# Performance work log

Hardware: AMD Instinct MI355X
Metric: run time of the kernel (lower is better)

## Reference

```python
import jax, jax.numpy as jnp
import numpy as np

N, E, D = 50000, 800000, 128
BN_EPS = 1e-5


def mish(x):
    return x * jnp.tanh(jax.nn.softplus(x))


def setup_inputs() -> dict:
    key = jax.random.key(0)
    ks = jax.random.split(key, 16)
    s = 1.0 / np.sqrt(D)
    s2 = 1.0 / np.sqrt(2 * D)
    # unique (row, col) edge pairs so the dense-adjacency edge norm reduces
    # exactly to conv_w[bond_type] + conv_b per edge
    rng = np.random.default_rng(0)
    codes = np.unique(rng.integers(0, N * N, size=2 * E, dtype=np.int64))[:E]
    edge_index = jnp.asarray(np.stack([codes // N, codes % N]), dtype=jnp.int32)
    bond_types = jnp.asarray(rng.integers(0, 4, size=E), dtype=jnp.int32)

    def nrm(k, shape, sc):
        return jax.random.normal(k, shape, jnp.float32) * sc

    return {
        "x": nrm(ks[0], (N, D), 1.0),
        "coords": nrm(ks[1], (N, 3), 1.0),
        "edge_index": edge_index,
        "bond_types": bond_types,
        # NodeFeaturePath
        "W_nb": nrm(ks[2], (2 * D, D), s2), "b_nb": jnp.zeros((D,), jnp.float32),
        "W_nout": nrm(ks[3], (D, D), s), "b_nout": jnp.zeros((D,), jnp.float32),
        # EdgeFeaturePath (1x1 conv over 4 bond-type channels -> scalar per edge)
        "conv_w": nrm(ks[4], (4,), 0.5), "conv_b": jnp.zeros((), jnp.float32),
        "W_el": nrm(ks[5], (2 * D, D), s2), "b_el": jnp.zeros((D,), jnp.float32),
        "W_eout": nrm(ks[6], (D, D), s), "b_eout": jnp.zeros((D,), jnp.float32),
        # StructuralFeaturePath
        "W_coord": nrm(ks[7], (2 * D, D), s2), "b_coord": jnp.zeros((D,), jnp.float32),
        "W_pair": nrm(ks[8], (D, D), s), "b_pair": jnp.zeros((D,), jnp.float32),
        "W_sout": nrm(ks[9], (2 * D, D), s2), "b_sout": jnp.zeros((D,), jnp.float32),
        # FeatureAggregation (att mode, all bias-free)
        "W_init": nrm(ks[10], (D, D), s),
        "feat_lin": nrm(ks[11], (3, D, D), s),
        "W_att": nrm(ks[12], (2 * D, D), s2),
        "W_agg": nrm(ks[13], (D, D), s),
        # BatchNorm (training mode)
        "gamma": jnp.ones((D,), jnp.float32), "beta": jnp.zeros((D,), jnp.float32),
    }


def _forward(x, coords, edge_index, bond_types,
             W_nb, b_nb, W_nout, b_nout,
             conv_w, conv_b, W_el, b_el, W_eout, b_eout,
             W_coord, b_coord, W_pair, b_pair, W_sout, b_sout,
             W_init, feat_lin, W_att, W_agg, gamma, beta):
    act = mish
    src, dst = edge_index[0], edge_index[1]  # PyG: x_j = x[src], x_i = x[dst]
    pair = jnp.concatenate([x[dst], x[src]], axis=1)  # [E, 2D] = [x_i, x_j]

    # --- node path ---
    msg = act(pair @ W_nb + b_nb)                                  # [E, D]
    P = jax.ops.segment_sum(msg, dst, num_segments=N)              # [N, D]
    f_node = act(P @ W_nout + b_nout)

    # --- edge path: 1x1 conv over one-hot bond-type adjacency == lookup ---
    norm_e = (conv_w[bond_types] + conv_b)[:, None]                # [E, 1]
    msg = act((norm_e * pair) @ W_el + b_el)
    P = jax.ops.segment_sum(msg, dst, num_segments=N)
    f_edge = act(P @ W_eout + b_eout)

    # --- struct path ---
    d2 = jnp.sum((coords[src] - coords[dst]) ** 2, axis=1, keepdims=True)  # [E,1]
    msg = (d2 * pair) @ W_coord + b_coord                          # no act in message
    Q = jax.ops.segment_sum(msg, dst, num_segments=N)
    Q = act(Q @ W_pair + b_pair)
    f_struct = act(jnp.concatenate([x, Q], axis=1) @ W_sout + b_sout)

    # --- attention aggregation over the 3 feature paths ---
    feat_stack = jnp.stack([f_node, f_edge, f_struct], axis=0)     # [3, N, D]
    lin_init = act(x @ W_init)[None]                               # [1, N, D] (broadcast of repeat)
    lin_feats = act(jnp.einsum('fnd,fde->fne', feat_stack, feat_lin))
    h = act(jnp.concatenate([jnp.broadcast_to(lin_init, lin_feats.shape), lin_feats], axis=2))
    e = h @ W_att                                                  # [3, N, D]
    a = jax.nn.softmax(e, axis=0)
    att = jnp.sum(a * feat_stack, axis=0)                          # einsum fnd,fnd->nd
    h_agg = att @ W_agg

    # --- batchnorm (training stats, biased var) + final activation ---
    mean = h_agg.mean(axis=0)
    var = h_agg.var(axis=0)
    h_bn = (h_agg - mean) / jnp.sqrt(var + BN_EPS) * gamma + beta
    return act(h_bn)  # final=False


def reference(x, coords, edge_index, bond_types,
              W_nb, b_nb, W_nout, b_nout,
              conv_w, conv_b, W_el, b_el, W_eout, b_eout,
              W_coord, b_coord, W_pair, b_pair, W_sout, b_sout,
              W_init, feat_lin, W_att, W_agg, gamma, beta):
    return _forward(x, coords, edge_index, bond_types,
                    W_nb, b_nb, W_nout, b_nout,
                    conv_w, conv_b, W_el, b_el, W_eout, b_eout,
                    W_coord, b_coord, W_pair, b_pair, W_sout, b_sout,
                    W_init, feat_lin, W_att, W_agg, gamma, beta)
```

## Files before the change

kernel.cpp:

```cpp
#include <hip/hip_runtime.h>
#include <math.h>

#define DD 128
#define LDSS 136
#define PLANE (16 * LDSS)
#define WT 16384

typedef __attribute__((ext_vector_type(8))) short bf16x8;
typedef __attribute__((ext_vector_type(4))) float f32x4;
typedef unsigned short u16;
typedef unsigned int u32;

__device__ __forceinline__ u16 f2bf(float f) {
    u32 u = __builtin_bit_cast(u32, f);
    u += 0x7fffu + ((u >> 16) & 1u);
    return (u16)(u >> 16);
}
__device__ __forceinline__ float bf2f(u16 h) {
    u32 u = ((u32)h) << 16;
    return __builtin_bit_cast(float, u);
}
__device__ __forceinline__ float mishf(float x) {
    float e = __expf(fminf(x, 15.0f));
    float n = e * (e + 2.0f);
    return x * n * __builtin_amdgcn_rcpf(n + 2.0f);
}
__device__ __forceinline__ void splitv(float v, u16& h, u16& l) {
    u32 u = __builtin_bit_cast(u32, v);
    h = (u16)(u >> 16);
    float r = v - __builtin_bit_cast(float, u & 0xffff0000u);
    l = (u16)(__builtin_bit_cast(u32, r) >> 16);
}

template<int NM>
__device__ __forceinline__ void gemm2(const bf16x8* ah, const bf16x8* al,
    const u16* __restrict__ Wh, const u16* __restrict__ Wl, int lane, int ntB, f32x4* acc)
{
#pragma unroll
    for (int kb = 0; kb < 4; kb++)
#pragma unroll
        for (int j = 0; j < 2; j++) {
            size_t boff = (((size_t)kb * 8 + ntB + j) * 64 + lane) * 8;
            bf16x8 bh = *(const bf16x8*)(Wh + boff);
            acc[j] = __builtin_amdgcn_mfma_f32_16x16x32_bf16(ah[kb], bh, acc[j], 0, 0, 0);
            if (NM >= 2) {
                bf16x8 bl = *(const bf16x8*)(Wl + boff);
                acc[j] = __builtin_amdgcn_mfma_f32_16x16x32_bf16(ah[kb], bl, acc[j], 0, 0, 0);
            }
            if (NM == 3)
                acc[j] = __builtin_amdgcn_mfma_f32_16x16x32_bf16(al[kb], bh, acc[j], 0, 0, 0);
        }
}

__device__ __forceinline__ void gemm2_dual(const bf16x8* a1, const bf16x8* a2,
    const u16* __restrict__ W1h, const u16* __restrict__ W1l,
    const u16* __restrict__ W2h, const u16* __restrict__ W2l,
    int lane, int ntB, f32x4* acc1, f32x4* acc2)
{
#pragma unroll
    for (int kb = 0; kb < 4; kb++)
#pragma unroll
        for (int j = 0; j < 2; j++) {
            size_t boff = (((size_t)kb * 8 + ntB + j) * 64 + lane) * 8;
            bf16x8 b1h = *(const bf16x8*)(W1h + boff);
            bf16x8 b1l = *(const bf16x8*)(W1l + boff);
            acc1[j] = __builtin_amdgcn_mfma_f32_16x16x32_bf16(a1[kb], b1h, acc1[j], 0, 0, 0);
            acc1[j] = __builtin_amdgcn_mfma_f32_16x16x32_bf16(a1[kb], b1l, acc1[j], 0, 0, 0);
            bf16x8 b2h = (W2h == W1h) ? b1h : *(const bf16x8*)(W2h + boff);
            bf16x8 b2l = (W2l == W1l) ? b1l : *(const bf16x8*)(W2l + boff);
            acc2[j] = __builtin_amdgcn_mfma_f32_16x16x32_bf16(a2[kb], b2h, acc2[j], 0, 0, 0);
            acc2[j] = __builtin_amdgcn_mfma_f32_16x16x32_bf16(a2[kb], b2l, acc2[j], 0, 0, 0);
        }
}

__device__ __forceinline__ void zero2(f32x4* acc) {
    f32x4 z4 = {0.f, 0.f, 0.f, 0.f};
    acc[0] = z4; acc[1] = z4;
}

__device__ __forceinline__ void frag_hi_global16(const u16* __restrict__ src, int row0,
                                                 int lm, int quad, int M, bf16x8* ah)
{
    int row = row0 + lm; if (row >= M) row = M - 1;
    const u16* p = src + (size_t)row * DD + quad * 8;
#pragma unroll
    for (int kb = 0; kb < 4; kb++) ah[kb] = *(const bf16x8*)(p + kb * 32);
}
__device__ __forceinline__ void frag_split_global16(const float* __restrict__ src, int row0,
                                                    int lm, int quad, int M, bf16x8* ah, bf16x8* al)
{
    int row = row0 + lm; if (row >= M) row = M - 1;
    const float* p = src + (size_t)row * DD + quad * 8;
#pragma unroll
    for (int kb = 0; kb < 4; kb++) {
        float tmp[8];
        *(float4*)tmp       = *(const float4*)(p + kb * 32);
        *(float4*)(tmp + 4) = *(const float4*)(p + kb * 32 + 4);
#pragma unroll
        for (int j = 0; j < 8; j++) { u16 h, l; splitv(tmp[j], h, l); ah[kb][j] = (short)h; al[kb][j] = (short)l; }
    }
}
__device__ __forceinline__ void frag_hi_plane16(const u16* P, int lm, int quad, bf16x8* ah)
{
    const u16* p = P + (size_t)lm * LDSS + quad * 8;
#pragma unroll
    for (int kb = 0; kb < 4; kb++) ah[kb] = *(const bf16x8*)(p + kb * 32);
}
__device__ __forceinline__ void frag_planes16(const u16* PH, const u16* PL, int lm, int quad,
                                              bf16x8* ah, bf16x8* al)
{
    const u16* ph = PH + (size_t)lm * LDSS + quad * 8;
    const u16* pl = PL + (size_t)lm * LDSS + quad * 8;
#pragma unroll
    for (int kb = 0; kb < 4; kb++) {
        ah[kb] = *(const bf16x8*)(ph + kb * 32);
        al[kb] = *(const bf16x8*)(pl + kb * 32);
    }
}

struct WSrc { const float* p[18]; };

__global__ __launch_bounds__(256) void prep_weights(WSrc ws, u16* __restrict__ Wh, u16* __restrict__ Wl)
{
    int mat = blockIdx.x >> 3, chunk = blockIdx.x & 7;
    int t = threadIdx.x;
    int tt = chunk * 4 + (t >> 6);
    int lane = t & 63;
    int kb = tt >> 3, nt = tt & 7;
    const float* __restrict__ src = ws.p[mat];
    size_t doff = (size_t)mat * WT + ((size_t)tt * 64 + lane) * 8;
    int srow = kb * 32 + ((lane >> 4) * 8);
    int scol = nt * 16 + (lane & 15);
    u16 th[8], tl[8];
#pragma unroll
    for (int j = 0; j < 8; j++) {
        float v = src[(srow + j) * DD + scol];
        u16 h = f2bf(v);
        th[j] = h;
        tl[j] = f2bf(v - bf2f(h));
    }
    *(bf16x8*)(Wh + doff) = *(bf16x8*)th;
    *(bf16x8*)(Wl + doff) = *(bf16x8*)tl;
}

__global__ __launch_bounds__(256, 4) void fronthist_kernel(
    const float* __restrict__ x, const u16* __restrict__ Wh, const u16* __restrict__ Wl,
    u16* __restrict__ G, u16* __restrict__ xWs,
    float* __restrict__ At, float* __restrict__ Bt, float* __restrict__ Ct,
    const int* __restrict__ ei, int* __restrict__ deg, int E, int M, int NBF)
{
    __shared__ u16 sP[3 * PLANE];
    const int t = threadIdx.x;
    if ((int)blockIdx.x >= NBF) {
        int e = ((int)blockIdx.x - NBF) * 256 + t;
        if (e < E) atomicAdd(&deg[ei[E + e]], 1);
        return;
    }
    u16 *P0 = sP, *P1 = sP + PLANE, *P2 = sP + 2 * PLANE;
    const int wave = t >> 6, lane = t & 63;
    const int lm = lane & 15, quad = lane >> 4;
    const int ntB = wave * 2;
    const int row0 = blockIdx.x * 16;

    bf16x8 ah[4], al[4];
    {
        int row = row0 + lm; if (row >= M) row = M - 1;
        const float* p = x + (size_t)row * DD + quad * 8;
#pragma unroll
        for (int kb = 0; kb < 4; kb++) {
            float tmp[8];
            *(float4*)tmp       = *(const float4*)(p + kb * 32);
            *(float4*)(tmp + 4) = *(const float4*)(p + kb * 32 + 4);
#pragma unroll
            for (int j = 0; j < 8; j++) {
                u16 h, l; splitv(tmp[j], h, l);
                ah[kb][j] = (short)h; al[kb][j] = (short)l;
                if (wave == 0) P0[lm * LDSS + kb * 32 + quad * 8 + j] = f2bf(tmp[j]);
            }
        }
    }
    {
        f32x4 acc[2]; zero2(acc);
        gemm2<1>(ah, ah, Wh + 1 * WT, Wh, lane, ntB, acc);
#pragma unroll
        for (int r = 0; r < 4; r++)
#pragma unroll
            for (int j = 0; j < 2; j++)
                P1[(quad * 4 + r) * LDSS + (ntB + j) * 16 + lm] = f2bf(acc[j][r]);
    }
    {
        f32x4 acc[2]; zero2(acc);
        gemm2<1>(ah, ah, Wh + 3 * WT, Wh, lane, ntB, acc);
#pragma unroll
        for (int r = 0; r < 4; r++)
#pragma unroll
            for (int j = 0; j < 2; j++)
                P2[(quad * 4 + r) * LDSS + (ntB + j) * 16 + lm] = f2bf(acc[j][r]);
    }
    __syncthreads();
#pragma unroll
    for (int i = 0; i < 4; i++) {
        int r = wave * 4 + i;
        int grow = row0 + r;
        if (grow >= M) continue;
        u16* gp = G + (size_t)grow * 384;
        *(u32*)(gp +       lane * 2) = *(const u32*)&P1[r * LDSS + lane * 2];
        *(u32*)(gp + 128 + lane * 2) = *(const u32*)&P2[r * LDSS + lane * 2];
        *(u32*)(gp + 256 + lane * 2) = *(const u32*)&P0[r * LDSS + lane * 2];
    }
    {
        f32x4 acc[2]; zero2(acc);
        gemm2<1>(ah, ah, Wh + 5 * WT, Wh, lane, ntB, acc);
#pragma unroll
        for (int r = 0; r < 4; r++) {
            int grow = row0 + quad * 4 + r;
            if (grow >= M) continue;
#pragma unroll
            for (int j = 0; j < 2; j++)
                xWs[(size_t)grow * DD + (ntB + j) * 16 + lm] = f2bf(acc[j][r]);
        }
    }
    {
        float* outs[3] = {At, Bt, Ct};
        const int mats[3] = {0, 2, 4};
#pragma unroll
        for (int wi = 0; wi < 3; wi++) {
            f32x4 acc[2]; zero2(acc);
            gemm2<3>(ah, al, Wh + (size_t)mats[wi] * WT, Wl + (size_t)mats[wi] * WT, lane, ntB, acc);
            float* out = outs[wi];
#pragma unroll
            for (int r = 0; r < 4; r++) {
                int grow = row0 + quad * 4 + r;
                if (grow >= M) continue;
#pragma unroll
                for (int j = 0; j < 2; j++)
                    out[(size_t)grow * DD + (ntB + j) * 16 + lm] = acc[j][r];
            }
        }
    }
}

__global__ __launch_bounds__(1024) void scan_kernel(const int* __restrict__ deg,
                                                    int* __restrict__ rowptr,
                                                    int* __restrict__ cursor, int N)
{
    __shared__ int sums[1024];
    const int CH = 52;
    int t = threadIdx.x;
    int base = t * CH;
    int local = 0;
#pragma unroll
    for (int i = 0; i < 13; i++) {
        int idx = base + i * 4;
        if (idx + 3 < N) {
            int4 v = *(const int4*)(deg + idx);
            local += v.x + v.y + v.z + v.w;
        } else {
            for (int k = 0; k < 4; k++) if (idx + k < N) local += deg[idx + k];
        }
    }
    sums[t] = local;
    __syncthreads();
    for (int off = 1; off < 1024; off <<= 1) {
        int v = sums[t];
        int u = (t >= off) ? sums[t - off] : 0;
        __syncthreads();
        sums[t] = v + u;
        __syncthreads();
    }
    int run = (t == 0) ? 0 : sums[t - 1];
    for (int i = 0; i < CH; i++) {
        int idx = base + i;
        if (idx < N) {
            rowptr[idx] = run;
            cursor[idx] = run;
            run += deg[idx];
        }
    }
    if (t == 1023) rowptr[N] = sums[1023];
}

__global__ __launch_bounds__(256) void scatter_kernel(
    const int* __restrict__ ei, const int* __restrict__ bond,
    const float* __restrict__ coords, int* __restrict__ cursor,
    int2* __restrict__ csr, int E)
{
    int e = blockIdx.x * 256 + threadIdx.x;
    if (e >= E) return;
    int src = ei[e], dst = ei[E + e];
    int pos = atomicAdd(&cursor[dst], 1);
    float dx = coords[src * 3 + 0] - coords[dst * 3 + 0];
    float dy = coords[src * 3 + 1] - coords[dst * 3 + 1];
    float dz = coords[src * 3 + 2] - coords[dst * 3 + 2];
    float d2 = dx * dx + dy * dy + dz * dz;
    csr[pos] = make_int2(src | (bond[e] << 20), __float_as_int(d2));
}

__global__ __launch_bounds__(256) void edge_agg(
    const float* __restrict__ At, const float* __restrict__ Bt,
    const u16* __restrict__ G,
    const int* __restrict__ rowptr, const int2* __restrict__ csr,
    const float* __restrict__ conv_w, const float* __restrict__ conv_b,
    const float* __restrict__ b_nb, const float* __restrict__ b_el,
    u16* __restrict__ Pn, u16* __restrict__ Pe, float* __restrict__ z,
    float* __restrict__ s_arr, int N)
{
    int wave = threadIdx.x >> 6;
    int lane = threadIdx.x & 63;
    int node = blockIdx.x * 4 + wave;
    if (node >= N) return;
    int c0 = lane * 2;
    float2 at = *(const float2*)(At + (size_t)node * DD + c0);
    float2 bt = *(const float2*)(Bt + (size_t)node * DD + c0);
    float cb = conv_b[0];
    float cw0 = conv_w[0] + cb, cw1 = conv_w[1] + cb, cw2 = conv_w[2] + cb, cw3 = conv_w[3] + cb;
    float bn0 = b_nb[c0], bn1 = b_nb[c0 + 1];
    float be0 = b_el[c0], be1 = b_el[c0 + 1];
    float accn0 = 0.f, accn1 = 0.f, acce0 = 0.f, acce1 = 0.f, accz0 = 0.f, accz1 = 0.f, ssum = 0.f;
    int beg = rowptr[node], end = rowptr[node + 1];

    auto consume = [&](int px, float d2, u32 ga, u32 gb, u32 gx) {
        int bondv = (px >> 20) & 3;
        float w = (bondv == 0) ? cw0 : (bondv == 1) ? cw1 : (bondv == 2) ? cw2 : cw3;
        float a0 = __builtin_bit_cast(float, ga << 16), a1 = __builtin_bit_cast(float, ga & 0xffff0000u);
        float b0 = __builtin_bit_cast(float, gb << 16), b1 = __builtin_bit_cast(float, gb & 0xffff0000u);
        float x0 = __builtin_bit_cast(float, gx << 16), x1 = __builtin_bit_cast(float, gx & 0xffff0000u);
        accn0 += mishf(at.x + a0 + bn0);
        accn1 += mishf(at.y + a1 + bn1);
        acce0 += mishf(w * (bt.x + b0) + be0);
        acce1 += mishf(w * (bt.y + b1) + be1);
        accz0 += d2 * x0;
        accz1 += d2 * x1;
        ssum += d2;
    };

    int k = beg;
    for (; k + 4 <= end; k += 4) {
        int2 pd0 = csr[k], pd1 = csr[k + 1], pd2 = csr[k + 2], pd3 = csr[k + 3];
        const u16* g0 = G + (size_t)(pd0.x & 0xFFFFF) * 384;
        const u16* g1 = G + (size_t)(pd1.x & 0xFFFFF) * 384;
        const u16* g2 = G + (size_t)(pd2.x & 0xFFFFF) * 384;
        const u16* g3 = G + (size_t)(pd3.x & 0xFFFFF) * 384;
        u32 ga0 = *(const u32*)(g0 + c0), gb0 = *(const u32*)(g0 + 128 + c0), gx0 = *(const u32*)(g0 + 256 + c0);
        u32 ga1 = *(const u32*)(g1 + c0), gb1 = *(const u32*)(g1 + 128 + c0), gx1 = *(const u32*)(g1 + 256 + c0);
        u32 ga2 = *(const u32*)(g2 + c0), gb2 = *(const u32*)(g2 + 128 + c0), gx2 = *(const u32*)(g2 + 256 + c0);
        u32 ga3 = *(const u32*)(g3 + c0), gb3 = *(const u32*)(g3 + 128 + c0), gx3 = *(const u32*)(g3 + 256 + c0);
        consume(pd0.x, __int_as_float(pd0.y), ga0, gb0, gx0);
        consume(pd1.x, __int_as_float(pd1.y), ga1, gb1, gx1);
        consume(pd2.x, __int_as_float(pd2.y), ga2, gb2, gx2);
        consume(pd3.x, __int_as_float(pd3.y), ga3, gb3, gx3);
    }
    for (; k < end; k++) {
        int2 pd = csr[k];
        const u16* gp = G + (size_t)(pd.x & 0xFFFFF) * 384;
        u32 ga = *(const u32*)(gp + c0);
        u32 gb = *(const u32*)(gp + 128 + c0);
        u32 gx = *(const u32*)(gp + 256 + c0);
        consume(pd.x, __int_as_float(pd.y), ga, gb, gx);
    }

    *(u32*)(Pn + (size_t)node * DD + c0) = (u32)f2bf(accn0) | ((u32)f2bf(accn1) << 16);
    *(u32*)(Pe + (size_t)node * DD + c0) = (u32)f2bf(acce0) | ((u32)f2bf(acce1) << 16);
    *(float2*)(z + (size_t)node * DD + c0) = make_float2(accz0, accz1);
    if (lane == 0) s_arr[node] = ssum;
}

__global__ __launch_bounds__(256, 4) void mega_kernel(
    const u16* __restrict__ Pn, const u16* __restrict__ Pe, const float* __restrict__ z,
    const float* __restrict__ Ct, const u16* __restrict__ xWs,
    const float* __restrict__ s_arr, const int* __restrict__ deg,
    const float* __restrict__ b_nout, const float* __restrict__ b_eout,
    const float* __restrict__ b_coord, const float* __restrict__ b_pair,
    const float* __restrict__ b_sout,
    const u16* __restrict__ Wh, const u16* __restrict__ Wl,
    float* __restrict__ hout, float* __restrict__ bnsums, int M)
{
    __shared__ u16 sP[4 * PLANE];
    u16 *PA = sP, *PB = sP + PLANE, *PC = sP + 2 * PLANE, *PD = sP + 3 * PLANE;
    const int t = threadIdx.x, wave = t >> 6, lane = t & 63;
    const int lm = lane & 15, quad = lane >> 4;
    const int ntB = wave * 2;
    const int row0 = blockIdx.x * 16;

    u32 f1p[4], f2p[4], f3p[4];
    float d1v[8], d2v[8];

    {
        bf16x8 an[4], ae[4];
        f32x4 accn[2], acce[2];
        frag_hi_global16(Pn, row0, lm, quad, M, an);
        frag_hi_global16(Pe, row0, lm, quad, M, ae);
        zero2(accn); zero2(acce);
        gemm2_dual(an, ae, Wh + 11 * WT, Wl + 11 * WT, Wh + 12 * WT, Wl + 12 * WT, lane, ntB, accn, acce);
#pragma unroll
        for (int r = 0; r < 4; r++) {
            u32 pkn = 0, pke = 0;
#pragma unroll
            for (int j = 0; j < 2; j++) {
                int col = (ntB + j) * 16 + lm;
                int lidx = (quad * 4 + r) * LDSS + col;
                u16 hn = f2bf(mishf(accn[j][r] + b_nout[col]));
                u16 he = f2bf(mishf(acce[j][r] + b_eout[col]));
                pkn |= ((u32)hn) << (16 * j);
                pke |= ((u32)he) << (16 * j);
                PA[lidx] = hn; PB[lidx] = he;
            }
            f1p[r] = pkn; f2p[r] = pke;
        }
        __syncthreads();
        frag_hi_plane16(PA, lm, quad, an);
        frag_hi_plane16(PB, lm, quad, ae);
        zero2(accn); zero2(acce);
        gemm2_dual(an, ae, Wh + 13 * WT, Wl + 13 * WT, Wh + 14 * WT, Wl + 14 * WT, lane, ntB, accn, acce);
#pragma unroll
        for (int r = 0; r < 4; r++)
#pragma unroll
            for (int j = 0; j < 2; j++) {
                int lidx = (quad * 4 + r) * LDSS + (ntB + j) * 16 + lm;
                PC[lidx] = f2bf(mishf(mishf(accn[j][r])));
                PD[lidx] = f2bf(mishf(mishf(acce[j][r])));
            }
        __syncthreads();
        frag_hi_plane16(PC, lm, quad, an);
        frag_hi_plane16(PD, lm, quad, ae);
        zero2(accn); zero2(acce);
        gemm2_dual(an, ae, Wh + 16 * WT, Wl + 16 * WT, Wh + 16 * WT, Wl + 16 * WT, lane, ntB, accn, acce);
#pragma unroll
        for (int r = 0; r < 4; r++)
#pragma unroll
            for (int j = 0; j < 2; j++) {
                d1v[r * 2 + j] = accn[j][r];
                d2v[r * 2 + j] = acce[j][r];
            }
    }

    bf16x8 ah[4], al[4];
    f32x4 acc[2];
    frag_split_global16(z, row0, lm, quad, M, ah, al);
    zero2(acc);
    gemm2<3>(ah, al, Wh + 8 * WT, Wl + 8 * WT, lane, ntB, acc);
#pragma unroll
    for (int r = 0; r < 4; r++) {
        int crow = row0 + quad * 4 + r; if (crow >= M) crow = M - 1;
        float sv = s_arr[crow];
        float dv = (float)deg[crow];
#pragma unroll
        for (int j = 0; j < 2; j++) {
            int col = (ntB + j) * 16 + lm;
            float v = acc[j][r] + sv * Ct[(size_t)crow * DD + col] + dv * b_coord[col];
            int lidx = (quad * 4 + r) * LDSS + col;
            u16 h, l; splitv(v, h, l); PA[lidx] = h; PB[lidx] = l;
        }
    }
    __syncthreads();
    frag_planes16(PA, PB, lm, quad, ah, al);
    zero2(acc);
    gemm2<3>(ah, al, Wh + 9 * WT, Wl + 9 * WT, lane, ntB, acc);
#pragma unroll
    for (int r = 0; r < 4; r++)
#pragma unroll
        for (int j = 0; j < 2; j++) {
            int col = (ntB + j) * 16 + lm;
            int lidx = (quad * 4 + r) * LDSS + col;
            u16 h, l; splitv(mishf(acc[j][r] + b_pair[col]), h, l); PC[lidx] = h; PD[lidx] = l;
        }
    __syncthreads();
    frag_planes16(PC, PD, lm, quad, ah, al);
    zero2(acc);
    gemm2<3>(ah, al, Wh + 10 * WT, Wl + 10 * WT, lane, ntB, acc);
#pragma unroll
    for (int r = 0; r < 4; r++) {
        int crow = row0 + quad * 4 + r; if (crow >= M) crow = M - 1;
        u32 pk = 0;
#pragma unroll
        for (int j = 0; j < 2; j++) {
            int col = (ntB + j) * 16 + lm;
            float v = mishf(acc[j][r] + bf2f(xWs[(size_t)crow * DD + col]) + b_sout[col]);
            u16 h, l; splitv(v, h, l);
            pk |= ((u32)f2bf(v)) << (16 * j);
            int lidx = (quad * 4 + r) * LDSS + col;
            PA[lidx] = h; PB[lidx] = l;
        }
        f3p[r] = pk;
    }
    __syncthreads();
    frag_planes16(PA, PB, lm, quad, ah, al);
    zero2(acc);
    gemm2<3>(ah, al, Wh + 15 * WT, Wl + 15 * WT, lane, ntB, acc);
#pragma unroll
    for (int r = 0; r < 4; r++)
#pragma unroll
        for (int j = 0; j < 2; j++) {
            int lidx = (quad * 4 + r) * LDSS + (ntB + j) * 16 + lm;
            u16 h, l; splitv(mishf(mishf(acc[j][r])), h, l); PC[lidx] = h; PD[lidx] = l;
        }
    __syncthreads();
    frag_planes16(PC, PD, lm, quad, ah, al);
    zero2(acc);
    gemm2<3>(ah, al, Wh + 16 * WT, Wl + 16 * WT, lane, ntB, acc);

#pragma unroll
    for (int r = 0; r < 4; r++)
#pragma unroll
        for (int j = 0; j < 2; j++) {
            int i = r * 2 + j;
            float x1 = d1v[i], x2 = d2v[i], x3 = acc[j][r];
            float m = fmaxf(fmaxf(x1, x2), x3);
            float p1 = __expf(x1 - m), p2 = __expf(x2 - m), p3 = __expf(x3 - m);
            float fv1 = bf2f((u16)(f1p[r] >> (16 * j)));
            float fv2 = bf2f((u16)(f2p[r] >> (16 * j)));
            float fv3 = bf2f((u16)(f3p[r] >> (16 * j)));
            float att = (p1 * fv1 + p2 * fv2 + p3 * fv3) * __builtin_amdgcn_rcpf(p1 + p2 + p3);
            int lidx = (quad * 4 + r) * LDSS + (ntB + j) * 16 + lm;
            u16 h, l; splitv(att, h, l); PA[lidx] = h; PB[lidx] = l;
        }
    __syncthreads();
    frag_planes16(PA, PB, lm, quad, ah, al);
    zero2(acc);
    gemm2<3>(ah, al, Wh + 17 * WT, Wl + 17 * WT, lane, ntB, acc);
    float s[2] = {0.f, 0.f}, q[2] = {0.f, 0.f};
#pragma unroll
    for (int r = 0; r < 4; r++) {
        int grow = row0 + quad * 4 + r;
        if (grow >= M) continue;
#pragma unroll
        for (int j = 0; j < 2; j++) {
            float v = acc[j][r];
            hout[(size_t)grow * DD + (ntB + j) * 16 + lm] = v;
            s[j] += v; q[j] += v * v;
        }
    }
    __syncthreads();
    float* red = (float*)sP;
    if (t < 128) { red[t] = 0.f; red[128 + t] = 0.f; }
    __syncthreads();
#pragma unroll
    for (int j = 0; j < 2; j++) {
        int col = (ntB + j) * 16 + lm;
        atomicAdd(&red[col], s[j]);
        atomicAdd(&red[128 + col], q[j]);
    }
    __syncthreads();
    if (t < 128) {
        atomicAdd(&bnsums[t], red[t]);
        atomicAdd(&bnsums[128 + t], red[128 + t]);
    }
}

__global__ void bn_finalize(const float* __restrict__ sums, const float* __restrict__ gamma,
                            const float* __restrict__ beta, float* __restrict__ scale,
                            float* __restrict__ shift, float n_inv)
{
    int c = threadIdx.x;
    float mean = sums[c] * n_inv;
    float var = sums[128 + c] * n_inv - mean * mean;
    float inv = rsqrtf(var + 1e-5f);
    float sc = gamma[c] * inv;
    scale[c] = sc;
    shift[c] = beta[c] - mean * sc;
}

__global__ __launch_bounds__(256) void bn_apply(float* __restrict__ h, const float* __restrict__ scale,
                                                const float* __restrict__ shift, size_t total4)
{
    size_t idx = (size_t)blockIdx.x * 256 + threadIdx.x;
    if (idx >= total4) return;
    size_t off = idx * 4;
    int c = (int)(off & 127);
    float4 v = *(const float4*)(h + off);
    float4 sc = *(const float4*)(scale + c);
    float4 sh = *(const float4*)(shift + c);
    v.x = mishf(v.x * sc.x + sh.x);
    v.y = mishf(v.y * sc.y + sh.y);
    v.z = mishf(v.z * sc.z + sh.z);
    v.w = mishf(v.w * sc.w + sh.w);
    *(float4*)(h + off) = v;
}

extern "C" void kernel_launch(void* const* d_in, const int* in_sizes, int n_in,
                              void* d_out, int out_size, void* d_ws, size_t ws_size,
                              hipStream_t stream)
{
    (void)n_in; (void)out_size; (void)ws_size;
    const float* x       = (const float*)d_in[0];
    const float* coords  = (const float*)d_in[1];
    const int*   ei      = (const int*)d_in[2];
    const int*   bond    = (const int*)d_in[3];
    const float* W_nb    = (const float*)d_in[4];
    const float* b_nb    = (const float*)d_in[5];
    const float* W_nout  = (const float*)d_in[6];
    const float* b_nout  = (const float*)d_in[7];
    const float* conv_w  = (const float*)d_in[8];
    const float* conv_b  = (const float*)d_in[9];
    const float* W_el    = (const float*)d_in[10];
    const float* b_el    = (const float*)d_in[11];
    const float* W_eout  = (const float*)d_in[12];
    const float* b_eout  = (const float*)d_in[13];
    const float* W_coord = (const float*)d_in[14];
    const float* b_coord = (const float*)d_in[15];
    const float* W_pair  = (const float*)d_in[16];
    const float* b_pair  = (const float*)d_in[17];
    const float* W_sout  = (const float*)d_in[18];
    const float* b_sout  = (const float*)d_in[19];
    const float* W_init  = (const float*)d_in[20];
    const float* feat_lin= (const float*)d_in[21];
    const float* W_att   = (const float*)d_in[22];
    const float* W_agg   = (const float*)d_in[23];
    const float* gamma   = (const float*)d_in[24];
    const float* beta    = (const float*)d_in[25];

    const int N = in_sizes[0] / DD;
    const int E = in_sizes[3];
    const size_t ND = (size_t)N * DD;
    const int SUB = DD * DD;
    const int NB16 = (N + 15) / 16;
    const int EB   = (E + 255) / 256;

    char* base = (char*)d_ws;
    size_t off = 0;
    auto alloc = [&](size_t bytes) -> char* {
        char* p = base + off;
        off = (off + bytes + 63) & ~(size_t)63;
        return p;
    };
    u16*   G    = (u16*)alloc((size_t)N * 384 * 2);
    u16*   xWs  = (u16*)alloc(ND * 2);
    float* At   = (float*)alloc(ND * 4);
    float* Bt   = (float*)alloc(ND * 4);
    float* Ct   = (float*)alloc(ND * 4);
    u16*   Pn   = (u16*)alloc(ND * 2);
    u16*   Pe   = (u16*)alloc(ND * 2);
    float* z    = (float*)alloc(ND * 4);
    u16*   Wh   = (u16*)alloc((size_t)18 * WT * 2);
    u16*   Wl   = (u16*)alloc((size_t)18 * WT * 2);
    int2*  csr  = (int2*)alloc((size_t)E * 8);
    int*   deg    = (int*)alloc((size_t)(N + 64) * 4);
    int*   rowptr = (int*)alloc((size_t)(N + 1) * 4);
    int*   cursor = (int*)alloc((size_t)N * 4);
    float* s_arr  = (float*)alloc((size_t)N * 4);
    float* bnsums  = (float*)alloc(256 * 4);
    float* bnscale = (float*)alloc(128 * 4);
    float* bnshift = (float*)alloc(128 * 4);

    float* hout = (float*)d_out;

    WSrc wsrc;
    wsrc.p[0] = W_nb;            wsrc.p[1] = W_nb + SUB;
    wsrc.p[2] = W_el;            wsrc.p[3] = W_el + SUB;
    wsrc.p[4] = W_coord;         wsrc.p[5] = W_sout;
    wsrc.p[6] = W_init;          wsrc.p[7] = W_att;
    wsrc.p[8] = W_coord + SUB;   wsrc.p[9] = W_pair;
    wsrc.p[10] = W_sout + SUB;   wsrc.p[11] = W_nout;
    wsrc.p[12] = W_eout;         wsrc.p[13] = feat_lin;
    wsrc.p[14] = feat_lin + SUB; wsrc.p[15] = feat_lin + 2 * SUB;
    wsrc.p[16] = W_att + SUB;    wsrc.p[17] = W_agg;

    const dim3 blk256(256);
    const size_t total4 = ND / 4;
    const dim3 gElem((unsigned)((total4 + 255) / 256));

    hipMemsetAsync(deg, 0, (size_t)N * 4, stream);
    hipMemsetAsync(bnsums, 0, 256 * 4, stream);

    prep_weights<<<dim3(18 * 8), blk256, 0, stream>>>(wsrc, Wh, Wl);
    fronthist_kernel<<<dim3(NB16 + EB), blk256, 0, stream>>>(x, Wh, Wl, G, xWs, At, Bt, Ct,
                                                             ei, deg, E, N, NB16);
    scan_kernel<<<1, 1024, 0, stream>>>(deg, rowptr, cursor, N);
    scatter_kernel<<<dim3(EB), blk256, 0, stream>>>(ei, bond, coords, cursor, csr, E);

    edge_agg<<<(N + 3) / 4, blk256, 0, stream>>>(At, Bt, G, rowptr, csr, conv_w, conv_b,
                                                 b_nb, b_el, Pn, Pe, z, s_arr, N);

    mega_kernel<<<NB16, blk256, 0, stream>>>(Pn, Pe, z, Ct, xWs, s_arr, deg,
                                             b_nout, b_eout, b_coord, b_pair, b_sout,
                                             Wh, Wl, hout, bnsums, N);

    bn_finalize<<<1, 128, 0, stream>>>(bnsums, gamma, beta, bnscale, bnshift, 1.0f / (float)N);
    bn_apply<<<gElem, blk256, 0, stream>>>(hout, bnscale, bnshift, total4);
}
```

Baseline: 613.8 us.

## Split node edges across two waves and add dual-accumulator MFMA chains

edge_agg now gives each node two waves that take alternating edges and combine their partial sums through shared memory, doubling the waves available to hide gather latency. Chosen GEMMs in mega_kernel use a second accumulator for odd k-blocks to break the serial MFMA dependency chain. mega_kernel's launch-bounds occupancy hint drops from 4 to 3 to leave room for the extra accumulator registers. Costs are a block-wide barrier, an LDS reduction in edge_agg, and possibly lower occupancy in mega_kernel.

New measurement: 623.0 us. Within noise of the previous version (+1.5%).

```diff
diff --git a/kernel.cpp b/kernel.cpp
--- a/kernel.cpp
+++ b/kernel.cpp
@@ -32,24 +32,36 @@
     l = (u16)(__builtin_bit_cast(u32, r) >> 16);
 }
 
-template<int NM>
+__device__ __forceinline__ void zero2(f32x4* acc) {
+    f32x4 z4 = {0.f, 0.f, 0.f, 0.f};
+    acc[0] = z4; acc[1] = z4;
+}
+
+template<int NM, bool SPLIT = false>
 __device__ __forceinline__ void gemm2(const bf16x8* ah, const bf16x8* al,
     const u16* __restrict__ Wh, const u16* __restrict__ Wl, int lane, int ntB, f32x4* acc)
 {
+    f32x4 accB[2];
+    if (SPLIT) zero2(accB);
 #pragma unroll
     for (int kb = 0; kb < 4; kb++)
 #pragma unroll
         for (int j = 0; j < 2; j++) {
             size_t boff = (((size_t)kb * 8 + ntB + j) * 64 + lane) * 8;
+            f32x4* ac = (SPLIT && (kb & 1)) ? accB : acc;
             bf16x8 bh = *(const bf16x8*)(Wh + boff);
-            acc[j] = __builtin_amdgcn_mfma_f32_16x16x32_bf16(ah[kb], bh, acc[j], 0, 0, 0);
+            ac[j] = __builtin_amdgcn_mfma_f32_16x16x32_bf16(ah[kb], bh, ac[j], 0, 0, 0);
             if (NM >= 2) {
                 bf16x8 bl = *(const bf16x8*)(Wl + boff);
-                acc[j] = __builtin_amdgcn_mfma_f32_16x16x32_bf16(ah[kb], bl, acc[j], 0, 0, 0);
+                ac[j] = __builtin_amdgcn_mfma_f32_16x16x32_bf16(ah[kb], bl, ac[j], 0, 0, 0);
             }
             if (NM == 3)
-                acc[j] = __builtin_amdgcn_mfma_f32_16x16x32_bf16(al[kb], bh, acc[j], 0, 0, 0);
-        }
+                ac[j] = __builtin_amdgcn_mfma_f32_16x16x32_bf16(al[kb], bh, ac[j], 0, 0, 0);
+        }
+    if (SPLIT) {
+        acc[0] += accB[0];
+        acc[1] += accB[1];
+    }
 }
 
 __device__ __forceinline__ void gemm2_dual(const bf16x8* a1, const bf16x8* a2,
@@ -73,11 +85,6 @@
         }
 }
 
-__device__ __forceinline__ void zero2(f32x4* acc) {
-    f32x4 z4 = {0.f, 0.f, 0.f, 0.f};
-    acc[0] = z4; acc[1] = z4;
-}
-
 __device__ __forceinline__ void frag_hi_global16(const u16* __restrict__ src, int row0,
                                                  int lm, int quad, int M, bf16x8* ah)
 {
@@ -305,19 +312,24 @@
     u16* __restrict__ Pn, u16* __restrict__ Pe, float* __restrict__ z,
     float* __restrict__ s_arr, int N)
 {
+    __shared__ float part[2][7][64];
     int wave = threadIdx.x >> 6;
     int lane = threadIdx.x & 63;
-    int node = blockIdx.x * 4 + wave;
-    if (node >= N) return;
+    int p = wave >> 1;
+    int s = wave & 1;
+    int node = blockIdx.x * 2 + p;
+    bool valid = node < N;
+    int nclamp = valid ? node : N - 1;
     int c0 = lane * 2;
-    float2 at = *(const float2*)(At + (size_t)node * DD + c0);
-    float2 bt = *(const float2*)(Bt + (size_t)node * DD + c0);
+    float2 at = *(const float2*)(At + (size_t)nclamp * DD + c0);
+    float2 bt = *(const float2*)(Bt + (size_t)nclamp * DD + c0);
     float cb = conv_b[0];
     float cw0 = conv_w[0] + cb, cw1 = conv_w[1] + cb, cw2 = conv_w[2] + cb, cw3 = conv_w[3] + cb;
     float bn0 = b_nb[c0], bn1 = b_nb[c0 + 1];
     float be0 = b_el[c0], be1 = b_el[c0 + 1];
     float accn0 = 0.f, accn1 = 0.f, acce0 = 0.f, acce1 = 0.f, accz0 = 0.f, accz1 = 0.f, ssum = 0.f;
-    int beg = rowptr[node], end = rowptr[node + 1];
+    int beg = 0, end = 0;
+    if (valid) { beg = rowptr[node]; end = rowptr[node + 1]; }
 
     auto consume = [&](int px, float d2, u32 ga, u32 gb, u32 gx) {
         int bondv = (px >> 20) & 3;
@@ -334,9 +346,9 @@
         ssum += d2;
     };
 
-    int k = beg;
-    for (; k + 4 <= end; k += 4) {
-        int2 pd0 = csr[k], pd1 = csr[k + 1], pd2 = csr[k + 2], pd3 = csr[k + 3];
+    int k = beg + s;
+    for (; k + 6 < end; k += 8) {
+        int2 pd0 = csr[k], pd1 = csr[k + 2], pd2 = csr[k + 4], pd3 = csr[k + 6];
         const u16* g0 = G + (size_t)(pd0.x & 0xFFFFF) * 384;
         const u16* g1 = G + (size_t)(pd1.x & 0xFFFFF) * 384;
         const u16* g2 = G + (size_t)(pd2.x & 0xFFFFF) * 384;
@@ -350,7 +362,7 @@
         consume(pd2.x, __int_as_float(pd2.y), ga2, gb2, gx2);
         consume(pd3.x, __int_as_float(pd3.y), ga3, gb3, gx3);
     }
-    for (; k < end; k++) {
+    for (; k < end; k += 2) {
         int2 pd = csr[k];
         const u16* gp = G + (size_t)(pd.x & 0xFFFFF) * 384;
         u32 ga = *(const u32*)(gp + c0);
@@ -359,13 +371,26 @@
         consume(pd.x, __int_as_float(pd.y), ga, gb, gx);
     }
 
-    *(u32*)(Pn + (size_t)node * DD + c0) = (u32)f2bf(accn0) | ((u32)f2bf(accn1) << 16);
-    *(u32*)(Pe + (size_t)node * DD + c0) = (u32)f2bf(acce0) | ((u32)f2bf(acce1) << 16);
-    *(float2*)(z + (size_t)node * DD + c0) = make_float2(accz0, accz1);
-    if (lane == 0) s_arr[node] = ssum;
-}
-
-__global__ __launch_bounds__(256, 4) void mega_kernel(
+    if (s == 1) {
+        part[p][0][lane] = accn0; part[p][1][lane] = accn1;
+        part[p][2][lane] = acce0; part[p][3][lane] = acce1;
+        part[p][4][lane] = accz0; part[p][5][lane] = accz1;
+        part[p][6][lane] = ssum;
+    }
+    __syncthreads();
+    if (s == 0 && valid) {
+        accn0 += part[p][0][lane]; accn1 += part[p][1][lane];
+        acce0 += part[p][2][lane]; acce1 += part[p][3][lane];
+        accz0 += part[p][4][lane]; accz1 += part[p][5][lane];
+        ssum  += part[p][6][lane];
+        *(u32*)(Pn + (size_t)node * DD + c0) = (u32)f2bf(accn0) | ((u32)f2bf(accn1) << 16);
+        *(u32*)(Pe + (size_t)node * DD + c0) = (u32)f2bf(acce0) | ((u32)f2bf(acce1) << 16);
+        *(float2*)(z + (size_t)node * DD + c0) = make_float2(accz0, accz1);
+        if (lane == 0) s_arr[node] = ssum;
+    }
+}
+
+__global__ __launch_bounds__(256, 3) void mega_kernel(
     const u16* __restrict__ Pn, const u16* __restrict__ Pe, const float* __restrict__ z,
     const float* __restrict__ Ct, const u16* __restrict__ xWs,
     const float* __restrict__ s_arr, const int* __restrict__ deg,
@@ -438,7 +463,7 @@
     f32x4 acc[2];
     frag_split_global16(z, row0, lm, quad, M, ah, al);
     zero2(acc);
-    gemm2<3>(ah, al, Wh + 8 * WT, Wl + 8 * WT, lane, ntB, acc);
+    gemm2<3, true>(ah, al, Wh + 8 * WT, Wl + 8 * WT, lane, ntB, acc);
 #pragma unroll
     for (int r = 0; r < 4; r++) {
         int crow = row0 + quad * 4 + r; if (crow >= M) crow = M - 1;
@@ -455,7 +480,7 @@
     __syncthreads();
     frag_planes16(PA, PB, lm, quad, ah, al);
     zero2(acc);
-    gemm2<3>(ah, al, Wh + 9 * WT, Wl + 9 * WT, lane, ntB, acc);
+    gemm2<3, true>(ah, al, Wh + 9 * WT, Wl + 9 * WT, lane, ntB, acc);
 #pragma unroll
     for (int r = 0; r < 4; r++)
 #pragma unroll
@@ -467,7 +492,7 @@
     __syncthreads();
     frag_planes16(PC, PD, lm, quad, ah, al);
     zero2(acc);
-    gemm2<3>(ah, al, Wh + 10 * WT, Wl + 10 * WT, lane, ntB, acc);
+    gemm2<3, true>(ah, al, Wh + 10 * WT, Wl + 10 * WT, lane, ntB, acc);
 #pragma unroll
     for (int r = 0; r < 4; r++) {
         int crow = row0 + quad * 4 + r; if (crow >= M) crow = M - 1;
@@ -486,7 +511,7 @@
     __syncthreads();
     frag_planes16(PA, PB, lm, quad, ah, al);
     zero2(acc);
-    gemm2<3>(ah, al, Wh + 15 * WT, Wl + 15 * WT, lane, ntB, acc);
+    gemm2<3, true>(ah, al, Wh + 15 * WT, Wl + 15 * WT, lane, ntB, acc);
 #pragma unroll
     for (int r = 0; r < 4; r++)
 #pragma unroll
@@ -497,7 +522,7 @@
     __syncthreads();
     frag_planes16(PC, PD, lm, quad, ah, al);
     zero2(acc);
-    gemm2<3>(ah, al, Wh + 16 * WT, Wl + 16 * WT, lane, ntB, acc);
+    gemm2<3, true>(ah, al, Wh + 16 * WT, Wl + 16 * WT, lane, ntB, acc);
 
 #pragma unroll
     for (int r = 0; r < 4; r++)
@@ -517,7 +542,7 @@
     __syncthreads();
     frag_planes16(PA, PB, lm, quad, ah, al);
     zero2(acc);
-    gemm2<3>(ah, al, Wh + 17 * WT, Wl + 17 * WT, lane, ntB, acc);
+    gemm2<3, true>(ah, al, Wh + 17 * WT, Wl + 17 * WT, lane, ntB, acc);
     float s[2] = {0.f, 0.f}, q[2] = {0.f, 0.f};
 #pragma unroll
     for (int r = 0; r < 4; r++) {
@@ -668,7 +693,7 @@
     scan_kernel<<<1, 1024, 0, stream>>>(deg, rowptr, cursor, N);
     scatter_kernel<<<dim3(EB), blk256, 0, stream>>>(ei, bond, coords, cursor, csr, E);
 
-    edge_agg<<<(N + 3) / 4, blk256, 0, stream>>>(At, Bt, G, rowptr, csr, conv_w, conv_b,
+    edge_agg<<<(N + 1) / 2, blk256, 0, stream>>>(At, Bt, G, rowptr, csr, conv_w, conv_b,
                                                  b_nb, b_el, Pn, Pe, z, s_arr, N);
 
     mega_kernel<<<NB16, blk256, 0, stream>>>(Pn, Pe, z, Ct, xWs, s_arr, deg,
```
